# Optimization experiments

Measured on AMD Instinct MI355X. Metric: run time of the kernel, lower is better.

Reference implementation:

```python
import jax, jax.numpy as jnp
import numpy as np

P = 25          # number of 3x3 positions on a 7x7 board (5x5 grid)
B = 8192        # batch
C_IN = 2        # input planes
DM = 128        # dim_middle
DF = 32         # dim_feature
CMAX = 127.0 / 128.0


def setup_inputs() -> dict:
    key = jax.random.key(0)
    ks = jax.random.split(key, 16)
    s = 0.05
    return {
        "x": jax.random.normal(ks[0], (B, C_IN, 7, 7), dtype=jnp.float32),
        # per-position (25 distinct towers) conv weights, torch layout (out,in,kh,kw)
        "W1": jax.random.normal(ks[1], (P, DM, C_IN, 2, 2), dtype=jnp.float32) * s,
        "b1": jax.random.normal(ks[2], (P, DM), dtype=jnp.float32) * s,
        "W2": jax.random.normal(ks[3], (P, DM, DM, 2, 2), dtype=jnp.float32) * s,
        "b2": jax.random.normal(ks[4], (P, DM), dtype=jnp.float32) * s,
        "W3": jax.random.normal(ks[5], (P, DM, DM), dtype=jnp.float32) * s,   # 1x1 conv
        "b3": jax.random.normal(ks[6], (P, DM), dtype=jnp.float32) * s,
        "W4": jax.random.normal(ks[7], (P, DF, DM), dtype=jnp.float32) * s,   # 1x1 conv, no act
        "b4": jax.random.normal(ks[8], (P, DF), dtype=jnp.float32) * s,
        # NNUE head MLP
        "fc1_w": jax.random.normal(ks[9], (DF, DF), dtype=jnp.float32) * s,
        "fc1_b": jax.random.normal(ks[10], (DF,), dtype=jnp.float32) * s,
        "fc2_w": jax.random.normal(ks[11], (DF, DF), dtype=jnp.float32) * s,
        "fc2_b": jax.random.normal(ks[12], (DF,), dtype=jnp.float32) * s,
        "fc3_w": jax.random.normal(ks[13], (1, DF), dtype=jnp.float32) * s,
        "fc3_b": jax.random.normal(ks[14], (1,), dtype=jnp.float32) * s,
    }


def _tower(x, W1, b1, W2, b2, W3, b3, W4, b4):
    # Gather the 25 3x3 patches -> [P, B, C, 3, 3] (fixed small Python loop over positions)
    patches = jnp.stack([x[:, :, y:y + 3, xx:xx + 3]
                         for y in range(5) for xx in range(5)], axis=0)
    # Conv1: 2x2 kernel on 3x3 -> 2x2 output, per-position weights, + ReLU
    h = jnp.stack([
        jnp.stack([
            jnp.einsum('pbcij,pocij->pbo', patches[..., i:i + 2, j:j + 2], W1)
            for j in range(2)], axis=-1)
        for i in range(2)], axis=-2)                       # [P, B, DM, 2, 2]
    h = jax.nn.relu(h + b1[:, None, :, None, None])
    # Conv2: 2x2 kernel on 2x2 -> 1x1, + ReLU
    h = jax.nn.relu(jnp.einsum('pbcij,pocij->pbo', h, W2) + b2[:, None, :])  # [P, B, DM]
    # Conv3: 1x1, + ReLU
    h = jax.nn.relu(jnp.einsum('pbc,poc->pbo', h, W3) + b3[:, None, :])
    # Conv4: 1x1, no activation, then clamp to [-1, 127/128]
    f = jnp.einsum('pbc,poc->pbo', h, W4) + b4[:, None, :]                   # [P, B, DF]
    f = jnp.clip(f, -1.0, CMAX)
    return f.sum(axis=0)                                    # [B, DF]


def reference(x, W1, b1, W2, b2, W3, b3, W4, b4,
              fc1_w, fc1_b, fc2_w, fc2_b, fc3_w, fc3_b):
    feature = _tower(x, W1, b1, W2, b2, W3, b3, W4, b4)
    v = jnp.clip(feature, 0.0, CMAX)
    # NNUE head: two clipped-ReLU linear layers + scalar output
    v = jnp.clip(v @ fc1_w.T + fc1_b, 0.0, CMAX)
    v = jnp.clip(v @ fc2_w.T + fc2_b, 0.0, CMAX)
    return v @ fc3_w.T + fc3_b                               # [B, 1]
```

## Files before the change

### kernel.cpp

```cpp
#include <hip/hip_runtime.h>
#include <hip/hip_bf16.h>


#define BATCH 8192
#define CMAXF 0.9921875f
#define NGRP 5
#define PPG 5

#define WF_TOTAL 2560000
#define PART_BYTE_OFF 5120000

using bf16x8 = __attribute__((ext_vector_type(8))) short;
using f32x4  = __attribute__((ext_vector_type(4))) float;

__device__ __forceinline__ unsigned short f2bf(float f) {
  union { float f; unsigned u; } v; v.f = f;
  unsigned u = v.u + 0x7fffu + ((v.u >> 16) & 1u);
  return (unsigned short)(u >> 16);
}

__device__ __forceinline__ f32x4 mfma16(bf16x8 a, bf16x8 b, f32x4 c) {
  return __builtin_amdgcn_mfma_f32_16x16x32_bf16(a, b, c, 0, 0, 0);
}

__device__ __forceinline__ void relu_pack2(f32x4 v, unsigned& lo, unsigned& hi) {
  union { __hip_bfloat162 h; unsigned u; } a_, b_;
  a_.h = __float22bfloat162_rn(make_float2(fmaxf(v[0], 0.f), fmaxf(v[1], 0.f)));
  b_.h = __float22bfloat162_rn(make_float2(fmaxf(v[2], 0.f), fmaxf(v[3], 0.f)));
  lo = a_.u; hi = b_.u;
}

__global__ __launch_bounds__(256) void prep_kernel(
    const float* __restrict__ W1, const float* __restrict__ b1,
    const float* __restrict__ W2, const float* __restrict__ W3,
    const float* __restrict__ W4, unsigned short* __restrict__ wf)
{
  int e4 = (blockIdx.x * 256 + threadIdx.x) * 4;
  if (e4 >= WF_TOTAL) return;
  const int j0 = e4 & 7;
  const int l = (e4 >> 3) & 63;
  const int f = (e4 >> 9) & 7;
  const int pq = e4 >> 12;
  const int p = pq / 25, q = pq - p * 25;
  const int g = l >> 4, l15 = l & 15;
  unsigned short vv[4];
#pragma unroll
  for (int i = 0; i < 4; ++i) {
    int j = j0 + i;
    float val = 0.f;
    if (q < 20) {
      int s = q / 5, rem = q - s * 5;
      if (rem == 0) {
        int o = f * 16 + l15;
        int kk = g * 8 + j;
        if (kk < 18) {
          int c = (kk >= 9) ? 1 : 0;
          int rr = kk - c * 9;
          int py = rr / 3, px = rr - py * 3;
          int si = s >> 1, sj = s & 1;
          int di = py - si, dj = px - sj;
          if (di >= 0 && di < 2 && dj >= 0 && dj < 2)
            val = W1[((p * 128 + o) * 2 + c) * 4 + di * 2 + dj];
        } else if (kk == 18) {
          val = b1[p * 128 + o];
        }
      } else {
        int kq = rem - 1;
        int o = f * 16 + l15;
        int c = kq * 32 + ((j >> 2) << 4) + g * 4 + (j & 3);
        val = W2[((p * 128 + o) * 128 + c) * 4 + s];
      }
    } else if (q < 24) {
      int kq = q - 20;
      int o = f * 16 + l15;
      int c = kq * 32 + ((j >> 2) << 4) + g * 4 + (j & 3);
      val = W3[(p * 128 + o) * 128 + c];
    } else {
      int nt = f >> 2, kq = f & 3;
      int o = nt * 16 + l15;
      int c = kq * 32 + ((j >> 2) << 4) + g * 4 + (j & 3);
      val = W4[(p * 32 + o) * 128 + c];
    }
    vv[i] = f2bf(val);
  }
  ushort4 st; st.x = vv[0]; st.y = vv[1]; st.z = vv[2]; st.w = vv[3];
  *(ushort4*)(wf + e4) = st;
}

#define BFRAG(pkm, kq) ({                                        \
  union { unsigned u[4]; bf16x8 v; } _bf;                        \
  _bf.u[0] = pkm[2*(kq)][0];   _bf.u[1] = pkm[2*(kq)][1];        \
  _bf.u[2] = pkm[2*(kq)+1][0]; _bf.u[3] = pkm[2*(kq)+1][1];      \
  _bf.v; })

__global__ __launch_bounds__(128, 2) void tower_kernel(
    const float* __restrict__ x,
    const float* __restrict__ b2v, const float* __restrict__ b3v,
    const float* __restrict__ b4v,
    const unsigned short* __restrict__ wf, float* __restrict__ part)
{
  __shared__ __align__(16) unsigned short xs[2][32 * 98];

  const int tid = threadIdx.x;
  const int l = tid & 63;
  const int wv = tid >> 6;
  const int l15 = l & 15;
  const int g = l >> 4;

  int bid = blockIdx.x;
  int lin = (bid & 7) * 80 + (bid >> 3);
  int grp = lin / 128;
  int btile = lin - grp * 128;
  const int R0 = btile * 64 + wv * 32;

  unsigned short* xsw = xs[wv];
  for (int idx = l; idx < 32 * 98; idx += 64)
    xsw[idx] = f2bf(x[(size_t)R0 * 98 + idx]);

  int kbase[8]; int kmode[8];
#pragma unroll
  for (int j = 0; j < 8; ++j) {
    int k = g * 8 + j;
    if (k < 18) {
      int c = (k >= 9) ? 1 : 0;
      int rr = k - c * 9;
      int py = rr / 3, px = rr - (rr / 3) * 3;
      kbase[j] = c * 49 + py * 7 + px;
      kmode[j] = 1;
    } else { kbase[j] = 0; kmode[j] = (k == 18) ? 2 : 0; }
  }

  const f32x4 zf = {0.f, 0.f, 0.f, 0.f};
  f32x4 facc[2][2] = {{zf, zf}, {zf, zf}};

  bf16x8 wA[8], wB[8];

#define PRE(DST, PN, QN)                                                          \
  {                                                                               \
    const unsigned short* s_ = wf + ((size_t)((PN) * 25 + (QN)) * 8) * 512 + l * 8; \
    _Pragma("unroll")                                                             \
    for (int f_ = 0; f_ < 8; ++f_) DST[f_] = *(const bf16x8*)(s_ + f_ * 512);     \
  }

#define L1PH(W)                                                                   \
  {                                                                               \
    __builtin_amdgcn_s_setprio(1);                                                \
    _Pragma("unroll")                                                             \
    for (int t_ = 0; t_ < 8; ++t_) {                                              \
      f32x4 c0_ = mfma16(W[t_], a1x[0], zf);                                      \
      f32x4 c1_ = mfma16(W[t_], a1x[1], zf);                                      \
      relu_pack2(c0_, pk[0][t_][0], pk[0][t_][1]);                                \
      relu_pack2(c1_, pk[1][t_][0], pk[1][t_][1]);                                \
    }                                                                             \
    __builtin_amdgcn_s_setprio(0);                                                \
  }

#define L2PH(W, KQ)                                                               \
  {                                                                               \
    bf16x8 bA_ = BFRAG(pk[0], KQ), bB_ = BFRAG(pk[1], KQ);                        \
    __builtin_amdgcn_s_setprio(1);                                                \
    _Pragma("unroll")                                                             \
    for (int t_ = 0; t_ < 8; ++t_) {                                              \
      acc[t_][0] = mfma16(W[t_], bA_, acc[t_][0]);                                \
      acc[t_][1] = mfma16(W[t_], bB_, acc[t_][1]);                                \
    }                                                                             \
    __builtin_amdgcn_s_setprio(0);                                                \
  }

  PRE(wA, grp * PPG, 0);

#pragma unroll 1
  for (int pp = 0; pp < PPG; ++pp) {
    const int p = grp * PPG + pp;
    const int y0 = p / 5;
    const int x0 = p - y0 * 5;
    const int poff = y0 * 7 + x0;

    bf16x8 a1x[2];
#pragma unroll
    for (int m = 0; m < 2; ++m) {
#pragma unroll
      for (int j = 0; j < 8; ++j) {
        unsigned short v = 0;
        if (kmode[j] == 1) v = xsw[(m * 16 + l15) * 98 + kbase[j] + poff];
        else if (kmode[j] == 2) v = 0x3F80;
        a1x[m][j] = (short)v;
      }
    }

    f32x4 acc[8][2];
#pragma unroll
    for (int t = 0; t < 8; ++t) {
      f32x4 b2 = *(const f32x4*)(b2v + p * 128 + t * 16 + g * 4);
      acc[t][0] = b2; acc[t][1] = b2;
    }

    unsigned pk[2][8][2];

#pragma unroll
    for (int s = 0; s < 4; ++s) {
      if ((s & 1) == 0) { PRE(wB, p, 5 * s + 1); L1PH(wA); }
      else              { PRE(wA, p, 5 * s + 1); L1PH(wB); }
#pragma unroll
      for (int kq = 0; kq < 4; ++kq) {
        if (((5 * s + 1 + kq) & 1) == 0) { PRE(wB, p, 5 * s + 2 + kq); L2PH(wA, kq); }
        else                             { PRE(wA, p, 5 * s + 2 + kq); L2PH(wB, kq); }
      }
    }

#pragma unroll
    for (int t = 0; t < 8; ++t) {
      f32x4 b3 = *(const f32x4*)(b3v + p * 128 + t * 16 + g * 4);
      relu_pack2(acc[t][0], pk[0][t][0], pk[0][t][1]);
      relu_pack2(acc[t][1], pk[1][t][0], pk[1][t][1]);
      acc[t][0] = b3; acc[t][1] = b3;
    }

#pragma unroll
    for (int kq = 0; kq < 4; ++kq) {
      if (((20 + kq) & 1) == 0) { PRE(wB, p, 21 + kq); L2PH(wA, kq); }
      else                      { PRE(wA, p, 21 + kq); L2PH(wB, kq); }
    }

#pragma unroll
    for (int t = 0; t < 8; ++t) {
      relu_pack2(acc[t][0], pk[0][t][0], pk[0][t][1]);
      relu_pack2(acc[t][1], pk[1][t][0], pk[1][t][1]);
    }

    f32x4 c4[2][2];
#pragma unroll
    for (int nt = 0; nt < 2; ++nt) {
      f32x4 b4 = *(const f32x4*)(b4v + p * 32 + nt * 16 + g * 4);
      c4[nt][0] = b4; c4[nt][1] = b4;
    }

    PRE(wB, p + 1, 0);
    {
      __builtin_amdgcn_s_setprio(1);
#pragma unroll
      for (int kq = 0; kq < 4; ++kq) {
        bf16x8 bA_ = BFRAG(pk[0], kq), bB_ = BFRAG(pk[1], kq);
#pragma unroll
        for (int nt = 0; nt < 2; ++nt) {
          c4[nt][0] = mfma16(wA[nt * 4 + kq], bA_, c4[nt][0]);
          c4[nt][1] = mfma16(wA[nt * 4 + kq], bB_, c4[nt][1]);
        }
      }
      __builtin_amdgcn_s_setprio(0);
#pragma unroll
      for (int nt = 0; nt < 2; ++nt) {
#pragma unroll
        for (int m = 0; m < 2; ++m) {
#pragma unroll
          for (int r = 0; r < 4; ++r) {
            float v = c4[nt][m][r];
            v = fminf(fmaxf(v, -1.f), CMAXF);
            facc[m][nt][r] += v;
          }
        }
      }
    }

#pragma unroll
    for (int f = 0; f < 8; ++f) wA[f] = wB[f];
  }
#undef PRE
#undef L1PH
#undef L2PH

#pragma unroll
  for (int m = 0; m < 2; ++m) {
#pragma unroll
    for (int nt = 0; nt < 2; ++nt) {
      *(f32x4*)(part + ((size_t)grp * BATCH + R0 + m * 16 + l15) * 32 + nt * 16 + g * 4)
          = facc[m][nt];
    }
  }
}

__global__ __launch_bounds__(256) void head_kernel(
    const float* __restrict__ part,
    const float* __restrict__ fc1w, const float* __restrict__ fc1b,
    const float* __restrict__ fc2w, const float* __restrict__ fc2b,
    const float* __restrict__ fc3w, const float* __restrict__ fc3b,
    float* __restrict__ out)
{
  const int lane = threadIdx.x & 63;
  const int o = lane & 31;
  const int half = lane >> 5;
  const int wave = threadIdx.x >> 6;
  const int row = blockIdx.x * 8 + wave * 2 + half;

  float feat = 0.f;
#pragma unroll
  for (int gi = 0; gi < NGRP; ++gi)
    feat += part[((size_t)gi * BATCH + row) * 32 + o];
  feat = feat < 0.f ? 0.f : (feat > CMAXF ? CMAXF : feat);

  float a = fc1b[o];
#pragma unroll
  for (int k = 0; k < 32; ++k)
    a += __shfl(feat, k, 32) * fc1w[o * 32 + k];
  a = a < 0.f ? 0.f : (a > CMAXF ? CMAXF : a);

  float b = fc2b[o];
#pragma unroll
  for (int k = 0; k < 32; ++k)
    b += __shfl(a, k, 32) * fc2w[o * 32 + k];
  b = b < 0.f ? 0.f : (b > CMAXF ? CMAXF : b);

  float c = b * fc3w[o];
#pragma unroll
  for (int m = 16; m >= 1; m >>= 1)
    c += __shfl_xor(c, m, 32);
  if (o == 0) out[row] = c + fc3b[0];
}

extern "C" void kernel_launch(void* const* d_in, const int* in_sizes, int n_in,
                              void* d_out, int out_size, void* d_ws, size_t ws_size,
                              hipStream_t stream) {
  const float* x    = (const float*)d_in[0];
  const float* W1   = (const float*)d_in[1];
  const float* b1   = (const float*)d_in[2];
  const float* W2   = (const float*)d_in[3];
  const float* b2   = (const float*)d_in[4];
  const float* W3   = (const float*)d_in[5];
  const float* b3   = (const float*)d_in[6];
  const float* W4   = (const float*)d_in[7];
  const float* b4   = (const float*)d_in[8];
  const float* fc1w = (const float*)d_in[9];
  const float* fc1b = (const float*)d_in[10];
  const float* fc2w = (const float*)d_in[11];
  const float* fc2b = (const float*)d_in[12];
  const float* fc3w = (const float*)d_in[13];
  const float* fc3b = (const float*)d_in[14];
  float* out = (float*)d_out;

  unsigned short* wf = (unsigned short*)d_ws;
  float* part = (float*)((char*)d_ws + PART_BYTE_OFF);

  prep_kernel<<<WF_TOTAL / 1024, 256, 0, stream>>>(W1, b1, W2, W3, W4, wf);
  tower_kernel<<<640, 128, 0, stream>>>(x, b2, b3, b4, wf, part);
  head_kernel<<<BATCH / 8, 256, 0, stream>>>(part, fc1w, fc1b, fc2w, fc2b, fc3w, fc3b, out);
}
```

Before: 87.22 us.

## Use one wave per block covering 64 batch rows to reuse weight fragments

The tower kernel now runs a single 64-lane wave per block that processes all 64 batch rows instead of two waves each handling 32 rows. Every weight fragment loaded from global memory is reused across four 16-row MFMA tiles rather than two, halving weight traffic per row. The cost is a much larger register footprint (accumulators 8x4, packed activations 4x8x2) and fewer waves per CU for latency hiding, with only 640 single-wave blocks on the device.

```diff
diff --git a/kernel.cpp b/kernel.cpp
--- a/kernel.cpp
+++ b/kernel.cpp
@@ -93,17 +93,15 @@
   _bf.u[2] = pkm[2*(kq)+1][0]; _bf.u[3] = pkm[2*(kq)+1][1];      \
   _bf.v; })
 
-__global__ __launch_bounds__(128, 2) void tower_kernel(
+__global__ __launch_bounds__(64, 1) void tower_kernel(
     const float* __restrict__ x,
     const float* __restrict__ b2v, const float* __restrict__ b3v,
     const float* __restrict__ b4v,
     const unsigned short* __restrict__ wf, float* __restrict__ part)
 {
-  __shared__ __align__(16) unsigned short xs[2][32 * 98];
-
-  const int tid = threadIdx.x;
-  const int l = tid & 63;
-  const int wv = tid >> 6;
+  __shared__ __align__(16) unsigned short xsw[64 * 98];
+
+  const int l = threadIdx.x;
   const int l15 = l & 15;
   const int g = l >> 4;
 
@@ -111,11 +109,11 @@
   int lin = (bid & 7) * 80 + (bid >> 3);
   int grp = lin / 128;
   int btile = lin - grp * 128;
-  const int R0 = btile * 64 + wv * 32;
-
-  unsigned short* xsw = xs[wv];
-  for (int idx = l; idx < 32 * 98; idx += 64)
+  const int R0 = btile * 64;
+
+  for (int idx = l; idx < 64 * 98; idx += 64)
     xsw[idx] = f2bf(x[(size_t)R0 * 98 + idx]);
+  __syncthreads();
 
   int kbase[8]; int kmode[8];
 #pragma unroll
@@ -131,7 +129,9 @@
   }
 
   const f32x4 zf = {0.f, 0.f, 0.f, 0.f};
-  f32x4 facc[2][2] = {{zf, zf}, {zf, zf}};
+  f32x4 facc[4][2];
+#pragma unroll
+  for (int m = 0; m < 4; ++m) { facc[m][0] = zf; facc[m][1] = zf; }
 
   bf16x8 wA[8], wB[8];
 
@@ -147,22 +147,26 @@
     __builtin_amdgcn_s_setprio(1);                                                \
     _Pragma("unroll")                                                             \
     for (int t_ = 0; t_ < 8; ++t_) {                                              \
-      f32x4 c0_ = mfma16(W[t_], a1x[0], zf);                                      \
-      f32x4 c1_ = mfma16(W[t_], a1x[1], zf);                                      \
-      relu_pack2(c0_, pk[0][t_][0], pk[0][t_][1]);                                \
-      relu_pack2(c1_, pk[1][t_][0], pk[1][t_][1]);                                \
+      _Pragma("unroll")                                                           \
+      for (int m_ = 0; m_ < 4; ++m_) {                                            \
+        f32x4 c_ = mfma16(W[t_], a1x[m_], zf);                                    \
+        relu_pack2(c_, pk[m_][t_][0], pk[m_][t_][1]);                             \
+      }                                                                           \
     }                                                                             \
     __builtin_amdgcn_s_setprio(0);                                                \
   }
 
 #define L2PH(W, KQ)                                                               \
   {                                                                               \
-    bf16x8 bA_ = BFRAG(pk[0], KQ), bB_ = BFRAG(pk[1], KQ);                        \
+    bf16x8 b0_ = BFRAG(pk[0], KQ), b1_ = BFRAG(pk[1], KQ);                        \
+    bf16x8 b2_ = BFRAG(pk[2], KQ), b3_ = BFRAG(pk[3], KQ);                        \
     __builtin_amdgcn_s_setprio(1);                                                \
     _Pragma("unroll")                                                             \
     for (int t_ = 0; t_ < 8; ++t_) {                                              \
-      acc[t_][0] = mfma16(W[t_], bA_, acc[t_][0]);                                \
-      acc[t_][1] = mfma16(W[t_], bB_, acc[t_][1]);                                \
+      acc[t_][0] = mfma16(W[t_], b0_, acc[t_][0]);                                \
+      acc[t_][1] = mfma16(W[t_], b1_, acc[t_][1]);                                \
+      acc[t_][2] = mfma16(W[t_], b2_, acc[t_][2]);                                \
+      acc[t_][3] = mfma16(W[t_], b3_, acc[t_][3]);                                \
     }                                                                             \
     __builtin_amdgcn_s_setprio(0);                                                \
   }
@@ -176,9 +180,9 @@
     const int x0 = p - y0 * 5;
     const int poff = y0 * 7 + x0;
 
-    bf16x8 a1x[2];
-#pragma unroll
-    for (int m = 0; m < 2; ++m) {
+    bf16x8 a1x[4];
+#pragma unroll
+    for (int m = 0; m < 4; ++m) {
 #pragma unroll
       for (int j = 0; j < 8; ++j) {
         unsigned short v = 0;
@@ -188,14 +192,15 @@
       }
     }
 
-    f32x4 acc[8][2];
+    f32x4 acc[8][4];
 #pragma unroll
     for (int t = 0; t < 8; ++t) {
       f32x4 b2 = *(const f32x4*)(b2v + p * 128 + t * 16 + g * 4);
-      acc[t][0] = b2; acc[t][1] = b2;
-    }
-
-    unsigned pk[2][8][2];
+#pragma unroll
+      for (int m = 0; m < 4; ++m) acc[t][m] = b2;
+    }
+
+    unsigned pk[4][8][2];
 
 #pragma unroll
     for (int s = 0; s < 4; ++s) {
@@ -211,9 +216,11 @@
 #pragma unroll
     for (int t = 0; t < 8; ++t) {
       f32x4 b3 = *(const f32x4*)(b3v + p * 128 + t * 16 + g * 4);
-      relu_pack2(acc[t][0], pk[0][t][0], pk[0][t][1]);
-      relu_pack2(acc[t][1], pk[1][t][0], pk[1][t][1]);
-      acc[t][0] = b3; acc[t][1] = b3;
+#pragma unroll
+      for (int m = 0; m < 4; ++m) {
+        relu_pack2(acc[t][m], pk[m][t][0], pk[m][t][1]);
+        acc[t][m] = b3;
+      }
     }
 
 #pragma unroll
@@ -224,15 +231,17 @@
 
 #pragma unroll
     for (int t = 0; t < 8; ++t) {
-      relu_pack2(acc[t][0], pk[0][t][0], pk[0][t][1]);
-      relu_pack2(acc[t][1], pk[1][t][0], pk[1][t][1]);
-    }
-
-    f32x4 c4[2][2];
+#pragma unroll
+      for (int m = 0; m < 4; ++m)
+        relu_pack2(acc[t][m], pk[m][t][0], pk[m][t][1]);
+    }
+
+    f32x4 c4[2][4];
 #pragma unroll
     for (int nt = 0; nt < 2; ++nt) {
       f32x4 b4 = *(const f32x4*)(b4v + p * 32 + nt * 16 + g * 4);
-      c4[nt][0] = b4; c4[nt][1] = b4;
+#pragma unroll
+      for (int m = 0; m < 4; ++m) c4[nt][m] = b4;
     }
 
     PRE(wB, p + 1, 0);
@@ -240,18 +249,21 @@
       __builtin_amdgcn_s_setprio(1);
 #pragma unroll
       for (int kq = 0; kq < 4; ++kq) {
-        bf16x8 bA_ = BFRAG(pk[0], kq), bB_ = BFRAG(pk[1], kq);
+        bf16x8 b0_ = BFRAG(pk[0], kq), b1_ = BFRAG(pk[1], kq);
+        bf16x8 b2_ = BFRAG(pk[2], kq), b3_ = BFRAG(pk[3], kq);
 #pragma unroll
         for (int nt = 0; nt < 2; ++nt) {
-          c4[nt][0] = mfma16(wA[nt * 4 + kq], bA_, c4[nt][0]);
-          c4[nt][1] = mfma16(wA[nt * 4 + kq], bB_, c4[nt][1]);
+          c4[nt][0] = mfma16(wA[nt * 4 + kq], b0_, c4[nt][0]);
+          c4[nt][1] = mfma16(wA[nt * 4 + kq], b1_, c4[nt][1]);
+          c4[nt][2] = mfma16(wA[nt * 4 + kq], b2_, c4[nt][2]);
+          c4[nt][3] = mfma16(wA[nt * 4 + kq], b3_, c4[nt][3]);
         }
       }
       __builtin_amdgcn_s_setprio(0);
 #pragma unroll
       for (int nt = 0; nt < 2; ++nt) {
 #pragma unroll
-        for (int m = 0; m < 2; ++m) {
+        for (int m = 0; m < 4; ++m) {
 #pragma unroll
           for (int r = 0; r < 4; ++r) {
             float v = c4[nt][m][r];
@@ -270,7 +282,7 @@
 #undef L2PH
 
 #pragma unroll
-  for (int m = 0; m < 2; ++m) {
+  for (int m = 0; m < 4; ++m) {
 #pragma unroll
     for (int nt = 0; nt < 2; ++nt) {
       *(f32x4*)(part + ((size_t)grp * BATCH + R0 + m * 16 + l15) * 32 + nt * 16 + g * 4)
@@ -341,6 +353,6 @@
   float* part = (float*)((char*)d_ws + PART_BYTE_OFF);
 
   prep_kernel<<<WF_TOTAL / 1024, 256, 0, stream>>>(W1, b1, W2, W3, W4, wf);
-  tower_kernel<<<640, 128, 0, stream>>>(x, b2, b3, b4, wf, part);
+  tower_kernel<<<640, 64, 0, stream>>>(x, b2, b3, b4, wf, part);
   head_kernel<<<BATCH / 8, 256, 0, stream>>>(part, fc1w, fc1b, fc2w, fc2b, fc3w, fc3b, out);
 }
```

Result: slower. 99.34 us (+13.9%).
